# Kernel tuning notes

Measured on AMD Instinct MI355X. Metric: run time of the kernel, lower is better.

## Reference

```python
import jax, jax.numpy as jnp
import numpy as np
from jax import lax

B, C, H, W = 32, 256, 56, 56
OUT_C, K, M = 256, 3, 8
STRIDE = (1, 1)
PADDING = ((1, 1), (1, 1))


def setup_inputs() -> dict:
    key = jax.random.key(0)
    ks = jax.random.split(key, 5)
    x = jax.random.normal(ks[0], (B, C, H, W), dtype=jnp.float32)
    # expert kernels: (M, out_C, in_C/groups, kh, kw), init like torch.randn*0.02
    weight = jax.random.normal(ks[1], (M, OUT_C, C, K, K), dtype=jnp.float32) * 0.02
    bias = jnp.zeros((M, OUT_C), dtype=jnp.float32)
    # gate Linear(in=C, out=M): torch stores weight as (out, in)
    bound = 1.0 / np.sqrt(C)
    gate_w = jax.random.uniform(ks[2], (M, C), minval=-bound, maxval=bound, dtype=jnp.float32)
    gate_b = jax.random.uniform(ks[3], (M,), minval=-bound, maxval=bound, dtype=jnp.float32)
    return {"x": x, "weight": weight, "bias": bias, "gate_w": gate_w, "gate_b": gate_b}


def reference(x, weight, bias, gate_w, gate_b):
    # global average pool -> gating
    gap = jnp.mean(x, axis=(2, 3))                         # (B, C)
    alpha = jax.nn.softmax(gap @ gate_w.T + gate_b, axis=1)  # (B, M)
    # per-sample combined kernels and biases
    kernels = jnp.einsum('bm,moikl->boikl', alpha, weight)  # (B, O, I, k, k)
    biases = alpha @ bias                                   # (B, O)

    def conv_one(xi, wi):
        # xi: (C,H,W), wi: (O,I,k,k)
        out = lax.conv_general_dilated(
            xi[None], wi,
            window_strides=STRIDE, padding=PADDING,
            dimension_numbers=('NCHW', 'OIHW', 'NCHW'))
        return out[0]  # (O, H, W)

    out = jax.vmap(conv_one)(x, kernels)                    # (B, O, H, W)
    return out + biases[:, :, None, None]
```

## Files before the change

### kernel.cpp

```cpp
#include <hip/hip_runtime.h>
#include <hip/hip_bf16.h>

#define B_    32
#define C_    256
#define HW_   3136
#define OC_   256
#define M_    8
#define KPB_  589824

typedef short v8s __attribute__((ext_vector_type(8)));
typedef float f32x4 __attribute__((ext_vector_type(4)));

union bf8pack { v8s v; __hip_bfloat16 h[8]; };

__device__ __forceinline__ void gll16(const short* src, short* dst) {
    __builtin_amdgcn_global_load_lds((const __attribute__((address_space(1))) void*)src,
                                     (__attribute__((address_space(3))) void*)dst, 16, 0, 0);
}

__global__ void zero_gap_kernel(float* __restrict__ gap) {
    gap[blockIdx.x * 256 + threadIdx.x] = 0.f;
}

__global__ __launch_bounds__(256) void xcast_kernel(const float* __restrict__ x,
                                                    short* __restrict__ xg,
                                                    float* __restrict__ gap) {
    __shared__ __hip_bfloat16 tile[64][65];
    int b = blockIdx.z, ct = blockIdx.y, pt = blockIdx.x;
    int p0 = pt*64, c0 = ct*64;
    int tp = threadIdx.x & 63, tc = threadIdx.x >> 6;
    const float* xb = x + ((size_t)b*C_ + c0) * HW_ + p0;
    #pragma unroll
    for (int j = 0; j < 16; ++j) {
        int cl = tc + j*4;
        float v = xb[(size_t)cl*HW_ + tp];
        tile[cl][tp] = __float2bfloat16(v);
        float s = v;
        #pragma unroll
        for (int off = 32; off; off >>= 1) s += __shfl_xor(s, off, 64);
        if (tp == 0) atomicAdd(&gap[b*C_ + c0 + cl], s);
    }
    __syncthreads();
    #pragma unroll
    for (int it = 0; it < 2; ++it) {
        int idx = it*256 + threadIdx.x;
        int px = idx >> 3, ck = idx & 7;
        bf8pack pk;
        #pragma unroll
        for (int j = 0; j < 8; ++j) pk.h[j] = tile[ck*8 + j][px];
        int c = c0 + ck*8;
        size_t dst = (((size_t)b*8 + (c >> 5))*HW_ + p0 + px)*32 + (c & 31);
        *(v8s*)(xg + dst) = pk.v;
    }
}

__global__ void alpha_kernel(const float* __restrict__ gap,
                             const float* __restrict__ gate_w,
                             const float* __restrict__ gate_b,
                             const float* __restrict__ bias,
                             float* __restrict__ alpha,
                             float* __restrict__ biasc) {
    int b = blockIdx.x, lane = threadIdx.x;
    const float inv = 1.0f / HW_;
    float g0 = gap[b*C_ + lane]*inv,       g1 = gap[b*C_ + 64 + lane]*inv;
    float g2 = gap[b*C_ + 128 + lane]*inv, g3 = gap[b*C_ + 192 + lane]*inv;
    float logit[M_];
    #pragma unroll
    for (int m = 0; m < M_; ++m) {
        const float* w = gate_w + m*C_;
        float s = g0*w[lane] + g1*w[64+lane] + g2*w[128+lane] + g3*w[192+lane];
        for (int off = 32; off; off >>= 1) s += __shfl_xor(s, off, 64);
        logit[m] = s + gate_b[m];
    }
    float mx = logit[0];
    #pragma unroll
    for (int m = 1; m < M_; ++m) mx = fmaxf(mx, logit[m]);
    float den = 0.f, e[M_];
    #pragma unroll
    for (int m = 0; m < M_; ++m) { e[m] = __expf(logit[m] - mx); den += e[m]; }
    float am[M_];
    #pragma unroll
    for (int m = 0; m < M_; ++m) am[m] = e[m] / den;
    if (lane < M_) alpha[b*M_ + lane] = am[lane];
    #pragma unroll
    for (int r = 0; r < 4; ++r) {
        int o = r*64 + lane;
        float s = 0.f;
        #pragma unroll
        for (int m = 0; m < M_; ++m) s += am[m] * bias[m*OC_ + o];
        biasc[b*OC_ + o] = s;
    }
}

__global__ __launch_bounds__(256) void combine_kernel(const float* __restrict__ weight,
                                                      const float* __restrict__ alpha,
                                                      short* __restrict__ wl) {
    __shared__ float as[B_*M_];
    as[threadIdx.x] = alpha[threadIdx.x];
    __syncthreads();
    int gc  = blockIdx.x*256 + threadIdx.x;
    int i8  = gc & 3;
    int o   = (gc >> 2) & 255;
    int t2  = gc >> 10;
    int tap = t2 % 9;
    int ib  = t2 / 9;
    int base = o*2304 + (ib*32 + i8*8)*9 + tap;
    float wv[M_][8];
    #pragma unroll
    for (int m = 0; m < M_; ++m)
        #pragma unroll
        for (int j = 0; j < 8; ++j)
            wv[m][j] = weight[(size_t)m*589824 + base + j*9];
    int b0 = blockIdx.y * 8;
    for (int b = b0; b < b0 + 8; ++b) {
        bf8pack pk;
        #pragma unroll
        for (int j = 0; j < 8; ++j) {
            float s = 0.f;
            #pragma unroll
            for (int m = 0; m < M_; ++m) s += as[b*M_+m] * wv[m][j];
            pk.h[j] = __float2bfloat16(s);
        }
        *(v8s*)(wl + (size_t)b*KPB_ + (size_t)gc*8) = pk.v;
    }
}

__global__ __launch_bounds__(256, 1) void conv_kernel(const short* __restrict__ xg,
                                                      const short* __restrict__ wl,
                                                      const float* __restrict__ biasc,
                                                      float* __restrict__ out) {
    __shared__ short smem[49152];

    const int wg  = blockIdx.x;
    const int swz = (wg & 7) * 56 + (wg >> 3);
    const int b   = swz / 14;
    const int pt  = swz - b * 14;

    const int tid = threadIdx.x;
    const int wave = tid >> 6, lane = tid & 63, q = lane >> 4, ln = lane & 15;
    const int P0 = pt * 224;

    const int DOFF[9] = {-57,-56,-55,-1,0,1,55,56,57};

    unsigned vmask[14];
    #pragma unroll
    for (int c = 0; c < 14; ++c) {
        int p = P0 + c*16 + ln;
        int h = p/56, w = p%56;
        unsigned m = 0;
        #pragma unroll
        for (int tap = 0; tap < 9; ++tap) {
            int h2 = h + tap/3 - 1, w2 = w + tap%3 - 1;
            if ((unsigned)h2 < 56u && (unsigned)w2 < 56u) m |= (1u << tap);
        }
        vmask[c] = m;
    }

    const short* wbase = wl + (size_t)b*KPB_ + tid*8;
    const short* xbase = xg + (size_t)(b*8)*HW_*32;

    auto stageA = [&](int kidx, int buf) {
        const short* src = wbase + (size_t)kidx*8192;
        #pragma unroll
        for (int r = 0; r < 4; ++r)
            gll16(src + r*2048, &smem[buf*8192 + tid*8 + r*2048]);
    };
    auto stageB = [&](int ib, int buf) {
        const short* src = xbase + ((long)ib*HW_ + P0 - 64)*32 + tid*8;
        short* dst = &smem[24576 + buf*12288 + tid*8];
        #pragma unroll
        for (int r = 0; r < 6; ++r) gll16(src + r*2048, dst + r*2048);
    };

    f32x4 acc[4][14];
    #pragma unroll
    for (int r = 0; r < 4; ++r)
        #pragma unroll
        for (int c = 0; c < 14; ++c) acc[r][c] = (f32x4){0.f,0.f,0.f,0.f};

    stageB(0, 0);
    stageA(0, 0);
    stageA(1, 1);

    const int a_lane_off = (wave*64 + ln)*32 + q*8;
    const int b_lane_off = 24576 + (64 + ln)*32 + q*8;
    const v8s vzero = {};

    for (int ib = 0; ib < 8; ++ib) {
        const short* bbuf = &smem[(ib & 1)*12288 + b_lane_off];
        #pragma unroll
        for (int tap = 0; tap < 9; ++tap) {
            const int k = ib*9 + tap;

            if (k == 71) {
                asm volatile("s_waitcnt vmcnt(0)" ::: "memory");
            } else if ((tap == 1 || tap == 2) && k <= 56) {
                asm volatile("s_waitcnt vmcnt(10)" ::: "memory");
            } else {
                asm volatile("s_waitcnt vmcnt(4)" ::: "memory");
            }
            __builtin_amdgcn_s_barrier();
            asm volatile("" ::: "memory");
            __builtin_amdgcn_sched_barrier(0);

            if (k + 2 < 72) stageA(k + 2, (k + 2) % 3);
            if (tap == 0 && ib < 7) stageB(ib + 1, (ib + 1) & 1);

            const short* am = &smem[(k % 3)*8192 + a_lane_off];
            v8s a[4];
            #pragma unroll
            for (int r = 0; r < 4; ++r) a[r] = *(const v8s*)(am + r*512);
            const short* bm = bbuf + DOFF[tap]*32;
            #pragma unroll
            for (int c = 0; c < 14; ++c) {
                v8s v = *(const v8s*)(bm + c*512);
                v8s bf = ((vmask[c] >> tap) & 1) ? v : vzero;
                #pragma unroll
                for (int r = 0; r < 4; ++r)
                    acc[r][c] = __builtin_amdgcn_mfma_f32_16x16x32_bf16(a[r], bf, acc[r][c], 0, 0, 0);
            }
        }
    }

    const int o0 = wave*64 + q*4;
    #pragma unroll
    for (int c = 0; c < 14; ++c) {
        int p = P0 + c*16 + ln;
        float* op = out + (size_t)b * OC_ * HW_ + p;
        #pragma unroll
        for (int r = 0; r < 4; ++r) {
            #pragma unroll
            for (int reg = 0; reg < 4; ++reg) {
                int o = o0 + r*16 + reg;
                op[(size_t)o * HW_] = acc[r][c][reg] + biasc[b*OC_ + o];
            }
        }
    }
}

extern "C" void kernel_launch(void* const* d_in, const int* in_sizes, int n_in,
                              void* d_out, int out_size, void* d_ws, size_t ws_size,
                              hipStream_t stream) {
    const float* x      = (const float*)d_in[0];
    const float* weight = (const float*)d_in[1];
    const float* bias   = (const float*)d_in[2];
    const float* gate_w = (const float*)d_in[3];
    const float* gate_b = (const float*)d_in[4];
    float* out = (float*)d_out;

    char* ws = (char*)d_ws;
    float* gap   = (float*)(ws);
    float* biasc = (float*)(ws + 32768);
    float* alpha = (float*)(ws + 65536);
    short* xg    = (short*)(ws + 131072);
    short* wl    = (short*)(ws + 51511296);

    zero_gap_kernel<<<32, 256, 0, stream>>>(gap);
    xcast_kernel   <<<dim3(49, 4, 32), 256, 0, stream>>>(x, xg, gap);
    alpha_kernel   <<<32,  64, 0, stream>>>(gap, gate_w, gate_b, bias, alpha, biasc);
    combine_kernel <<<dim3(288, 4), 256, 0, stream>>>(weight, alpha, wl);
    conv_kernel    <<<448, 256, 0, stream>>>(xg, wl, biasc, out);
}
```

Measured before the change: 450.8 us.

## Shrink conv LDS to fit two blocks per CU and restructure staging waits

The conv kernel drops the double-buffered input tile for a single buffer, which cuts LDS so two workgroups can share a CU (launch bounds 2). Each wave now stages its own slice of the weight tile, so most taps need only a per-wave vmcnt wait instead of a block barrier; a full barrier pair remains around each input-tile reload. Masked taps read a zero row in LDS instead of using a register select, and MFMA sections run at raised priority. The combine kernel now loops over all 32 batches per block with fewer blocks, and the conv kernel risks register spilling under the tighter launch bound and more exposed input-tile loads.

```diff
diff --git a/kernel.cpp b/kernel.cpp
--- a/kernel.cpp
+++ b/kernel.cpp
@@ -111,8 +111,7 @@
         #pragma unroll
         for (int j = 0; j < 8; ++j)
             wv[m][j] = weight[(size_t)m*589824 + base + j*9];
-    int b0 = blockIdx.y * 8;
-    for (int b = b0; b < b0 + 8; ++b) {
+    for (int b = 0; b < B_; ++b) {
         bf8pack pk;
         #pragma unroll
         for (int j = 0; j < 8; ++j) {
@@ -125,11 +124,11 @@
     }
 }
 
-__global__ __launch_bounds__(256, 1) void conv_kernel(const short* __restrict__ xg,
+__global__ __launch_bounds__(256, 2) void conv_kernel(const short* __restrict__ xg,
                                                       const short* __restrict__ wl,
                                                       const float* __restrict__ biasc,
                                                       float* __restrict__ out) {
-    __shared__ short smem[49152];
+    __shared__ short smem[36880];
 
     const int wg  = blockIdx.x;
     const int swz = (wg & 7) * 56 + (wg >> 3);
@@ -156,18 +155,18 @@
         vmask[c] = m;
     }
 
-    const short* wbase = wl + (size_t)b*KPB_ + tid*8;
+    const short* wbase = wl + (size_t)b*KPB_ + wave*2048 + lane*8;
     const short* xbase = xg + (size_t)(b*8)*HW_*32;
 
     auto stageA = [&](int kidx, int buf) {
         const short* src = wbase + (size_t)kidx*8192;
-        #pragma unroll
-        for (int r = 0; r < 4; ++r)
-            gll16(src + r*2048, &smem[buf*8192 + tid*8 + r*2048]);
+        short* dst = &smem[buf*8192 + wave*2048 + lane*8];
+        #pragma unroll
+        for (int r = 0; r < 4; ++r) gll16(src + r*512, dst + r*512);
     };
-    auto stageB = [&](int ib, int buf) {
+    auto stageB = [&](int ib) {
         const short* src = xbase + ((long)ib*HW_ + P0 - 64)*32 + tid*8;
-        short* dst = &smem[24576 + buf*12288 + tid*8];
+        short* dst = &smem[24576 + tid*8];
         #pragma unroll
         for (int r = 0; r < 6; ++r) gll16(src + r*2048, dst + r*2048);
     };
@@ -178,47 +177,62 @@
         #pragma unroll
         for (int c = 0; c < 14; ++c) acc[r][c] = (f32x4){0.f,0.f,0.f,0.f};
 
-    stageB(0, 0);
+    if (tid == 0) { *(v8s*)&smem[36864] = (v8s){}; *(v8s*)&smem[36872] = (v8s){}; }
+
+    stageB(0);
     stageA(0, 0);
     stageA(1, 1);
-
-    const int a_lane_off = (wave*64 + ln)*32 + q*8;
-    const int b_lane_off = 24576 + (64 + ln)*32 + q*8;
-    const v8s vzero = {};
+    asm volatile("s_waitcnt vmcnt(4) lgkmcnt(0)" ::: "memory");
+    __builtin_amdgcn_s_barrier();
+    asm volatile("" ::: "memory");
+
+    const int a_off = wave*2048 + ln*32 + q*8;
+    int bcol[14];
+    #pragma unroll
+    for (int c = 0; c < 14; ++c) bcol[c] = 24576 + (64 + ln)*32 + q*8 + c*512;
+    const int zoff = 36864;
 
     for (int ib = 0; ib < 8; ++ib) {
-        const short* bbuf = &smem[(ib & 1)*12288 + b_lane_off];
         #pragma unroll
         for (int tap = 0; tap < 9; ++tap) {
             const int k = ib*9 + tap;
 
-            if (k == 71) {
-                asm volatile("s_waitcnt vmcnt(0)" ::: "memory");
-            } else if ((tap == 1 || tap == 2) && k <= 56) {
-                asm volatile("s_waitcnt vmcnt(10)" ::: "memory");
+            if (tap == 0 && ib > 0) {
+                __builtin_amdgcn_s_barrier();
+                asm volatile("" ::: "memory");
+                stageB(ib);
+                stageA(k + 2, (tap + 2) % 3);
+                asm volatile("s_waitcnt vmcnt(4)" ::: "memory");
+                __builtin_amdgcn_s_barrier();
+                asm volatile("" ::: "memory");
             } else {
-                asm volatile("s_waitcnt vmcnt(4)" ::: "memory");
+                if (k + 2 < 72) {
+                    stageA(k + 2, (tap + 2) % 3);
+                    asm volatile("s_waitcnt vmcnt(8)" ::: "memory");
+                } else if (k == 70) {
+                    asm volatile("s_waitcnt vmcnt(4)" ::: "memory");
+                } else {
+                    asm volatile("s_waitcnt vmcnt(0)" ::: "memory");
+                }
             }
-            __builtin_amdgcn_s_barrier();
-            asm volatile("" ::: "memory");
             __builtin_amdgcn_sched_barrier(0);
 
-            if (k + 2 < 72) stageA(k + 2, (k + 2) % 3);
-            if (tap == 0 && ib < 7) stageB(ib + 1, (ib + 1) & 1);
-
-            const short* am = &smem[(k % 3)*8192 + a_lane_off];
             v8s a[4];
             #pragma unroll
-            for (int r = 0; r < 4; ++r) a[r] = *(const v8s*)(am + r*512);
-            const short* bm = bbuf + DOFF[tap]*32;
+            for (int r = 0; r < 4; ++r)
+                a[r] = *(const v8s*)&smem[(tap % 3)*8192 + a_off + r*512];
+
+            const int doff32 = DOFF[tap]*32;
+            __builtin_amdgcn_s_setprio(1);
             #pragma unroll
             for (int c = 0; c < 14; ++c) {
-                v8s v = *(const v8s*)(bm + c*512);
-                v8s bf = ((vmask[c] >> tap) & 1) ? v : vzero;
+                int off = ((vmask[c] >> tap) & 1) ? (bcol[c] + doff32) : zoff;
+                v8s v = *(const v8s*)&smem[off];
                 #pragma unroll
                 for (int r = 0; r < 4; ++r)
-                    acc[r][c] = __builtin_amdgcn_mfma_f32_16x16x32_bf16(a[r], bf, acc[r][c], 0, 0, 0);
+                    acc[r][c] = __builtin_amdgcn_mfma_f32_16x16x32_bf16(a[r], v, acc[r][c], 0, 0, 0);
             }
+            __builtin_amdgcn_s_setprio(0);
         }
     }
 
@@ -258,6 +272,6 @@
     zero_gap_kernel<<<32, 256, 0, stream>>>(gap);
     xcast_kernel   <<<dim3(49, 4, 32), 256, 0, stream>>>(x, xg, gap);
     alpha_kernel   <<<32,  64, 0, stream>>>(gap, gate_w, gate_b, bias, alpha, biasc);
-    combine_kernel <<<dim3(288, 4), 256, 0, stream>>>(weight, alpha, wl);
+    combine_kernel <<<288, 256, 0, stream>>>(weight, alpha, wl);
     conv_kernel    <<<448, 256, 0, stream>>>(xg, wl, biasc, out);
 }
```

Result: slower. 808.0 us (+79.2%).

## Halve conv pixel tile, load weights straight to registers, run two blocks per CU

Applied to the files above, without the earlier changes.

Each conv workgroup now covers 112 pixels instead of 224, so the grid doubles to 896 blocks and launch bounds allow two blocks per CU. Weight fragments are loaded straight from global memory into double-buffered registers instead of being staged through LDS, which cuts LDS use and removes the per-tap barriers. Out-of-bounds taps read a zeroed LDS slot instead of using a select. The combine kernel now loops over all batches in one block dimension. In exchange, weights are reused across fewer pixels per block, which doubles global weight traffic, and register-latency hiding now depends on the extra occupancy.

```diff
diff --git a/kernel.cpp b/kernel.cpp
--- a/kernel.cpp
+++ b/kernel.cpp
@@ -111,8 +111,7 @@
         #pragma unroll
         for (int j = 0; j < 8; ++j)
             wv[m][j] = weight[(size_t)m*589824 + base + j*9];
-    int b0 = blockIdx.y * 8;
-    for (int b = b0; b < b0 + 8; ++b) {
+    for (int b = 0; b < B_; ++b) {
         bf8pack pk;
         #pragma unroll
         for (int j = 0; j < 8; ++j) {
@@ -125,26 +124,26 @@
     }
 }
 
-__global__ __launch_bounds__(256, 1) void conv_kernel(const short* __restrict__ xg,
+__global__ __launch_bounds__(256, 2) void conv_kernel(const short* __restrict__ xg,
                                                       const short* __restrict__ wl,
                                                       const float* __restrict__ biasc,
                                                       float* __restrict__ out) {
-    __shared__ short smem[49152];
+    __shared__ short smem[16400];
 
     const int wg  = blockIdx.x;
-    const int swz = (wg & 7) * 56 + (wg >> 3);
-    const int b   = swz / 14;
-    const int pt  = swz - b * 14;
+    const int swz = (wg & 7) * 112 + (wg >> 3);
+    const int b   = swz / 28;
+    const int pt  = swz - b * 28;
 
     const int tid = threadIdx.x;
     const int wave = tid >> 6, lane = tid & 63, q = lane >> 4, ln = lane & 15;
-    const int P0 = pt * 224;
+    const int P0 = pt * 112;
 
     const int DOFF[9] = {-57,-56,-55,-1,0,1,55,56,57};
 
-    unsigned vmask[14];
-    #pragma unroll
-    for (int c = 0; c < 14; ++c) {
+    unsigned vmask[7];
+    #pragma unroll
+    for (int c = 0; c < 7; ++c) {
         int p = P0 + c*16 + ln;
         int h = p/56, w = p%56;
         unsigned m = 0;
@@ -156,75 +155,66 @@
         vmask[c] = m;
     }
 
-    const short* wbase = wl + (size_t)b*KPB_ + tid*8;
+    const short* wbase = wl + (size_t)b*KPB_ + (wave*64 + ln)*32 + q*8;
     const short* xbase = xg + (size_t)(b*8)*HW_*32;
 
-    auto stageA = [&](int kidx, int buf) {
-        const short* src = wbase + (size_t)kidx*8192;
-        #pragma unroll
-        for (int r = 0; r < 4; ++r)
-            gll16(src + r*2048, &smem[buf*8192 + tid*8 + r*2048]);
-    };
     auto stageB = [&](int ib, int buf) {
         const short* src = xbase + ((long)ib*HW_ + P0 - 64)*32 + tid*8;
-        short* dst = &smem[24576 + buf*12288 + tid*8];
-        #pragma unroll
-        for (int r = 0; r < 6; ++r) gll16(src + r*2048, dst + r*2048);
+        short* dst = &smem[buf*8192 + tid*8];
+        #pragma unroll
+        for (int r = 0; r < 4; ++r) gll16(src + r*2048, dst + r*2048);
     };
 
-    f32x4 acc[4][14];
+    v8s areg[2][4];
+    auto loadA = [&](int kidx, v8s (&dst)[4]) {
+        const short* src = wbase + (size_t)kidx*8192;
+        #pragma unroll
+        for (int r = 0; r < 4; ++r) dst[r] = *(const v8s*)(src + r*512);
+    };
+
+    f32x4 acc[4][7];
     #pragma unroll
     for (int r = 0; r < 4; ++r)
         #pragma unroll
-        for (int c = 0; c < 14; ++c) acc[r][c] = (f32x4){0.f,0.f,0.f,0.f};
+        for (int c = 0; c < 7; ++c) acc[r][c] = (f32x4){0.f,0.f,0.f,0.f};
+
+    if (tid == 0) *(v8s*)&smem[16384] = (v8s){};
 
     stageB(0, 0);
-    stageA(0, 0);
-    stageA(1, 1);
-
-    const int a_lane_off = (wave*64 + ln)*32 + q*8;
-    const int b_lane_off = 24576 + (64 + ln)*32 + q*8;
-    const v8s vzero = {};
-
-    for (int ib = 0; ib < 8; ++ib) {
-        const short* bbuf = &smem[(ib & 1)*12288 + b_lane_off];
-        #pragma unroll
-        for (int tap = 0; tap < 9; ++tap) {
-            const int k = ib*9 + tap;
-
-            if (k == 71) {
-                asm volatile("s_waitcnt vmcnt(0)" ::: "memory");
-            } else if ((tap == 1 || tap == 2) && k <= 56) {
-                asm volatile("s_waitcnt vmcnt(10)" ::: "memory");
-            } else {
-                asm volatile("s_waitcnt vmcnt(4)" ::: "memory");
+    loadA(0, areg[0]);
+
+    const int bcol0 = (64 + ln)*32 + q*8;
+
+    for (int ib2 = 0; ib2 < 4; ++ib2) {
+        #pragma unroll
+        for (int ibu = 0; ibu < 2; ++ibu) {
+            const int ib = ib2*2 + ibu;
+            __syncthreads();
+            if (ib < 7) stageB(ib + 1, ibu ^ 1);
+
+            #pragma unroll
+            for (int tap = 0; tap < 9; ++tap) {
+                const int k = ib*9 + tap;
+                if (k + 1 < 72) loadA(k + 1, areg[(ibu + tap + 1) & 1]);
+                const v8s* A = areg[(ibu + tap) & 1];
+                const int base = ibu*8192 + bcol0 + DOFF[tap]*32;
+                __builtin_amdgcn_s_setprio(1);
+                #pragma unroll
+                for (int c = 0; c < 7; ++c) {
+                    int off = ((vmask[c] >> tap) & 1) ? (base + c*512) : 16384;
+                    v8s v = *(const v8s*)&smem[off];
+                    #pragma unroll
+                    for (int r = 0; r < 4; ++r)
+                        acc[r][c] = __builtin_amdgcn_mfma_f32_16x16x32_bf16(A[r], v, acc[r][c], 0, 0, 0);
+                }
+                __builtin_amdgcn_s_setprio(0);
             }
-            __builtin_amdgcn_s_barrier();
-            asm volatile("" ::: "memory");
-            __builtin_amdgcn_sched_barrier(0);
-
-            if (k + 2 < 72) stageA(k + 2, (k + 2) % 3);
-            if (tap == 0 && ib < 7) stageB(ib + 1, (ib + 1) & 1);
-
-            const short* am = &smem[(k % 3)*8192 + a_lane_off];
-            v8s a[4];
-            #pragma unroll
-            for (int r = 0; r < 4; ++r) a[r] = *(const v8s*)(am + r*512);
-            const short* bm = bbuf + DOFF[tap]*32;
-            #pragma unroll
-            for (int c = 0; c < 14; ++c) {
-                v8s v = *(const v8s*)(bm + c*512);
-                v8s bf = ((vmask[c] >> tap) & 1) ? v : vzero;
-                #pragma unroll
-                for (int r = 0; r < 4; ++r)
-                    acc[r][c] = __builtin_amdgcn_mfma_f32_16x16x32_bf16(a[r], bf, acc[r][c], 0, 0, 0);
-            }
         }
     }
 
     const int o0 = wave*64 + q*4;
     #pragma unroll
-    for (int c = 0; c < 14; ++c) {
+    for (int c = 0; c < 7; ++c) {
         int p = P0 + c*16 + ln;
         float* op = out + (size_t)b * OC_ * HW_ + p;
         #pragma unroll
@@ -258,6 +248,6 @@
     zero_gap_kernel<<<32, 256, 0, stream>>>(gap);
     xcast_kernel   <<<dim3(49, 4, 32), 256, 0, stream>>>(x, xg, gap);
     alpha_kernel   <<<32,  64, 0, stream>>>(gap, gate_w, gate_b, bias, alpha, biasc);
-    combine_kernel <<<dim3(288, 4), 256, 0, stream>>>(weight, alpha, wl);
-    conv_kernel    <<<448, 256, 0, stream>>>(xg, wl, biasc, out);
-}
+    combine_kernel <<<288, 256, 0, stream>>>(weight, alpha, wl);
+    conv_kernel    <<<896, 256, 0, stream>>>(xg, wl, biasc, out);
+}
```

Measured after the change: 506.1 us. +12.3%, slower.
